# Kernel tuning notes

Hardware: AMD Instinct MI355X
Metric: run time of the kernel (lower is better)

Reference implementation:

```python
import jax, jax.numpy as jnp
import numpy as np

B, S, D = 2, 2048, 1024
QH, KVH, DH = 16, 4, 64
TOP_K = 128
ROPE_BASE = 10000.0


def _rope(x):
    # x: [B, H, S, DH]; standard LLaMA-style rotate-half RoPE, no freq scaling
    half = DH // 2
    inv_freq = 1.0 / (ROPE_BASE ** (jnp.arange(half, dtype=jnp.float32) / half))
    ang = jnp.arange(S, dtype=jnp.float32)[:, None] * inv_freq[None, :]  # [S, half]
    cos, sin = jnp.cos(ang), jnp.sin(ang)
    x1, x2 = x[..., :half], x[..., half:]
    return jnp.concatenate([x1 * cos - x2 * sin, x2 * cos + x1 * sin], axis=-1)


def setup_inputs() -> dict:
    key = jax.random.key(0)
    ks = jax.random.split(key, 5)
    return {
        "x": jax.random.normal(ks[0], (B, S, D), dtype=jnp.float32),
        "Wq": jax.random.normal(ks[1], (QH * DH, D), dtype=jnp.float32) * 0.02,
        "Wk": jax.random.normal(ks[2], (KVH * DH, D), dtype=jnp.float32) * 0.02,
        "Wv": jax.random.normal(ks[3], (KVH * DH, D), dtype=jnp.float32) * 0.02,
        "Wo": jax.random.normal(ks[4], (D, QH * DH), dtype=jnp.float32) * 0.02,
    }


def reference(x, Wq, Wk, Wv, Wo):
    # projections (Linear, no bias): y = x @ W.T
    q = (x @ Wq.T).reshape(B, S, QH, DH).transpose(0, 2, 1, 3)   # [B,QH,S,DH]
    k = (x @ Wk.T).reshape(B, S, KVH, DH).transpose(0, 2, 1, 3)  # [B,KVH,S,DH]
    v = (x @ Wv.T).reshape(B, S, KVH, DH).transpose(0, 2, 1, 3)
    q = _rope(q)
    k = _rope(k)
    # repeat_kv: GQA expand kv heads to q heads
    rep = QH // KVH
    k = jnp.repeat(k, rep, axis=1)
    v = jnp.repeat(v, rep, axis=1)
    scores = jnp.einsum("bhqd,bhkd->bhqk", q, k) / np.sqrt(DH)  # [B,QH,S,S]
    causal = jnp.triu(jnp.ones((S, S), dtype=bool), k=1)
    scores = jnp.where(causal, -jnp.inf, scores)
    # top-k masking before softmax: keep entries >= per-row k-th largest score
    top_vals = jax.lax.top_k(scores, TOP_K)[0]        # [B,QH,S,TOP_K]
    thr = top_vals[..., -1:]
    scores = jnp.where(scores < thr, -jnp.inf, scores)
    w = jax.nn.softmax(scores, axis=-1)
    out = jnp.einsum("bhqk,bhkd->bhqd", w, v)         # [B,QH,S,DH]
    out = out.transpose(0, 2, 1, 3).reshape(B, S, QH * DH)
    return out @ Wo.T
```

## Files before the change

kernel.cpp:

```cpp
#include <hip/hip_runtime.h>
#include <hip/hip_bf16.h>
#include <hip/hip_fp16.h>
#include <math.h>

constexpr int cB   = 2;
constexpr int cS   = 2048;
constexpr int cD   = 1024;
constexpr int cQH  = 16;
constexpr int cKVH = 4;
constexpr int cDH  = 64;
constexpr int cTOPK = 128;
constexpr int cM   = cB * cS;
constexpr int cNB  = cS / 64;
constexpr int cLSZ = 384;

constexpr int cTI  = 8;
constexpr int cSTR = 130;

constexpr int cNQ  = cQH * cDH;
constexpr int cNK  = cKVH * cDH;
constexpr int cNQKV = cNQ + 2 * cNK;

typedef __attribute__((ext_vector_type(8))) short short8;
typedef __attribute__((ext_vector_type(4))) float floatx4;
typedef _Float16 half8 __attribute__((ext_vector_type(8)));

__device__ inline ushort f2bf(float f) {
    unsigned u = __float_as_uint(f);
    return (ushort)((u + 0x7FFFu + ((u >> 16) & 1u)) >> 16);
}

__device__ __forceinline__ void glds16(const ushort* g, ushort* l) {
    __builtin_amdgcn_global_load_lds(
        (const __attribute__((address_space(1))) unsigned int*)g,
        (__attribute__((address_space(3))) unsigned int*)l, 16, 0, 0);
}

constexpr int cE0 = cM * cD;
constexpr int cE1 = cE0 + cNQ * cD;
constexpr int cE2 = cE1 + cNK * cD;
constexpr int cE3 = cE2 + cNK * cD;
constexpr int cE4 = cE3 + cD * cQH * cDH;

__global__ void cast_all_bf16(const float* __restrict__ x,
                              const float* __restrict__ wq,
                              const float* __restrict__ wk,
                              const float* __restrict__ wv,
                              const float* __restrict__ wo,
                              ushort* __restrict__ dst) {
    const int i4 = (blockIdx.x * blockDim.x + threadIdx.x) * 4;
    if (i4 >= cE4) return;
    const float* s;
    int off;
    if (i4 < cE0)      { s = x;  off = i4; }
    else if (i4 < cE1) { s = wq; off = i4 - cE0; }
    else if (i4 < cE2) { s = wk; off = i4 - cE1; }
    else if (i4 < cE3) { s = wv; off = i4 - cE2; }
    else               { s = wo; off = i4 - cE3; }
    const float4 v = *(const float4*)(s + off);
    ushort4 r;
    r.x = f2bf(v.x); r.y = f2bf(v.y); r.z = f2bf(v.z); r.w = f2bf(v.w);
    *(ushort4*)(dst + i4) = r;
}

__global__ __launch_bounds__(256) void gemm_bf16_bt(
        const ushort* __restrict__ A, const ushort* __restrict__ W,
        float* __restrict__ C, int M, int N, int K) {
    __shared__ ushort AsL[128 * 32];
    __shared__ ushort BsL[128 * 32];

    const int tid  = threadIdx.x;
    const int lane = tid & 63;
    const int w    = tid >> 6;
    const int wm   = (w & 1) * 64;
    const int wn   = (w >> 1) * 64;
    const int m0   = blockIdx.y * 128;
    const int n0   = blockIdx.x * 128;
    const int quad = lane >> 4;
    const int l16  = lane & 15;

    int r0, q0, r1, q1;
    {
        const int g5 = (w * 128 + lane) & 31;
        const int b4 = (g5 >> 4) & 1, b3 = (g5 >> 3) & 1, b2 = (g5 >> 2) & 1;
        const int b1 = (g5 >> 1) & 1, b0 = g5 & 1;
        r0 = ((w * 128 + lane) >> 5) * 8 + ((b4 << 2) | (b3 << 1) | (b2 ^ b4));
        q0 = ((b1 ^ b3) << 1) | (b0 ^ b2 ^ b4);
    }
    {
        const int gI = w * 128 + 64 + lane;
        const int g5 = gI & 31;
        const int b4 = (g5 >> 4) & 1, b3 = (g5 >> 3) & 1, b2 = (g5 >> 2) & 1;
        const int b1 = (g5 >> 1) & 1, b0 = g5 & 1;
        r1 = (gI >> 5) * 8 + ((b4 << 2) | (b3 << 1) | (b2 ^ b4));
        q1 = ((b1 ^ b3) << 1) | (b0 ^ b2 ^ b4);
    }
    const size_t aOff0 = (size_t)(m0 + r0) * K + q0 * 8;
    const size_t aOff1 = (size_t)(m0 + r1) * K + q1 * 8;
    const size_t bOff0 = (size_t)(n0 + r0) * K + q0 * 8;
    const size_t bOff1 = (size_t)(n0 + r1) * K + q1 * 8;
    ushort* ldsA0 = AsL + w * 1024;
    ushort* ldsA1 = AsL + w * 1024 + 512;
    ushort* ldsB0 = BsL + w * 1024;
    ushort* ldsB1 = BsL + w * 1024 + 512;

    int eA[4], eB[4];
    #pragma unroll
    for (int mi = 0; mi < 4; ++mi) {
        const int rr = wm + mi * 16 + l16;
        eA[mi] = (((rr >> 3) * 32) + ((4 * (rr & 7) + quad) ^ (rr & 7))) * 8;
    }
    #pragma unroll
    for (int ni = 0; ni < 4; ++ni) {
        const int rn = wn + ni * 16 + l16;
        eB[ni] = (((rn >> 3) * 32) + ((4 * (rn & 7) + quad) ^ (rn & 7))) * 8;
    }

    floatx4 acc[4][4];
    #pragma unroll
    for (int mi = 0; mi < 4; ++mi)
        #pragma unroll
        for (int ni = 0; ni < 4; ++ni)
            acc[mi][ni] = (floatx4){0.f, 0.f, 0.f, 0.f};

    for (int k0 = 0; k0 < K; k0 += 32) {
        glds16(A + aOff0 + k0, ldsA0);
        glds16(A + aOff1 + k0, ldsA1);
        glds16(W + bOff0 + k0, ldsB0);
        glds16(W + bOff1 + k0, ldsB1);
        __syncthreads();

        short8 af[4], bf[4];
        #pragma unroll
        for (int mi = 0; mi < 4; ++mi)
            af[mi] = *(const short8*)(AsL + eA[mi]);
        #pragma unroll
        for (int ni = 0; ni < 4; ++ni)
            bf[ni] = *(const short8*)(BsL + eB[ni]);
        #pragma unroll
        for (int mi = 0; mi < 4; ++mi)
            #pragma unroll
            for (int ni = 0; ni < 4; ++ni)
                acc[mi][ni] = __builtin_amdgcn_mfma_f32_16x16x32_bf16(
                    af[mi], bf[ni], acc[mi][ni], 0, 0, 0);
        __syncthreads();
    }

    #pragma unroll
    for (int mi = 0; mi < 4; ++mi)
        #pragma unroll
        for (int ni = 0; ni < 4; ++ni)
            #pragma unroll
            for (int r = 0; r < 4; ++r) {
                const int row = m0 + wm + mi * 16 + quad * 4 + r;
                const int col = n0 + wn + ni * 16 + l16;
                C[(size_t)row * N + col] = acc[mi][ni][r];
            }
}

__global__ void rope_cast_f16(const float* __restrict__ src,
                              ushort* __restrict__ dst, int H, int total,
                              float scale, int srcStride) {
    int idx = blockIdx.x * blockDim.x + threadIdx.x;
    if (idx >= total) return;
    const int d   = idx & 31;
    const int h   = (idx >> 5) % H;
    const int row = idx / (32 * H);
    const int s   = row % cS;
    const float inv_freq = powf(10000.0f, -(float)d / 32.0f);
    const float ang = (float)s * inv_freq;
    const float c  = cosf(ang);
    const float si = sinf(ang);
    const float* p = src + (size_t)row * srcStride + (size_t)h * cDH;
    const float x1 = p[d];
    const float x2 = p[d + 32];
    const float r1 = (x1 * c - x2 * si) * scale;
    const float r2 = (x2 * c + x1 * si) * scale;
    ushort* o = dst + (size_t)row * H * cDH + (size_t)h * cDH;
    o[d]      = __builtin_bit_cast(ushort, (_Float16)r1);
    o[d + 32] = __builtin_bit_cast(ushort, (_Float16)r2);
}

__global__ void cast_f32_f16_strided(const float* __restrict__ src,
                                     ushort* __restrict__ dst,
                                     int total, int cols, int srcStride) {
    const int i4 = (blockIdx.x * blockDim.x + threadIdx.x) * 4;
    if (i4 >= total) return;
    const int row = i4 / cols;
    const int col = i4 - row * cols;
    const float4 v = *(const float4*)(src + (size_t)row * srcStride + col);
    ushort4 r;
    r.x = __builtin_bit_cast(ushort, (_Float16)v.x);
    r.y = __builtin_bit_cast(ushort, (_Float16)v.y);
    r.z = __builtin_bit_cast(ushort, (_Float16)v.z);
    r.w = __builtin_bit_cast(ushort, (_Float16)v.w);
    *(ushort4*)(dst + i4) = r;
}

__device__ inline unsigned fmap(float f) {
    unsigned u = __float_as_uint(f);
    return (u & 0x80000000u) ? ~u : (u | 0x80000000u);
}
__device__ inline float funmap(unsigned u) {
    unsigned v = (u & 0x80000000u) ? (u & 0x7FFFFFFFu) : ~u;
    return __uint_as_float(v);
}

__global__ __launch_bounds__(512) void attn_tile_kernel(
        const ushort* __restrict__ qf, const ushort* __restrict__ kf,
        const ushort* __restrict__ vf, ushort* __restrict__ out) {
    extern __shared__ char smem[];
    unsigned* stg = (unsigned*)smem;
    unsigned* klA = (unsigned*)smem;
    int*      jlA = (int*)(klA + cTI * cLSZ);

    const int lane = threadIdx.x & 63;
    const int wv   = __builtin_amdgcn_readfirstlane(threadIdx.x >> 6);

    const int x  = blockIdx.x;
    const int it = (cS / cTI - 1) - (x >> 5);
    const int bh = x & 31;
    const int h  = bh & 15;
    const int b  = bh >> 4;
    const int kvh = h >> 2;
    const int i0  = it * cTI;

    const size_t bS = (size_t)b * cS;
    const int l16   = lane & 15;
    const int quad  = lane >> 4;
    const int jperm = ((lane & 3) << 4) + (lane >> 2);
    const int i     = i0 + wv;

    const ushort* qp = qf + ((bS + i0 + (l16 & 7)) * cQH + h) * cDH + quad * 8;
    const half8 a0h = __builtin_bit_cast(half8, *(const uint4*)qp);
    const half8 a1h = __builtin_bit_cast(half8, *(const uint4*)(qp + 32));

    unsigned key[cNB];
    #pragma unroll
    for (int jb = 0; jb < cNB; ++jb) key[jb] = 0u;

    const int nk16   = ((i0 + cTI - 1) >> 4) + 1;
    const int nchunk = (nk16 + 7) >> 3;

    uint4 pb0, pb1;
    if (wv < nk16) {
        const ushort* kp = kf + ((bS + (wv << 4) + l16) * cKVH + kvh) * cDH + quad * 8;
        pb0 = *(const uint4*)kp;
        pb1 = *(const uint4*)(kp + 32);
    }

    #pragma unroll
    for (int c = 0; c < 16; ++c) {
        if (c >= nchunk) break;
        const int  kb16  = (c << 3) + wv;
        const bool valid = (kb16 < nk16);
        const uint4 b0 = pb0, b1 = pb1;
        const int  kb16n = ((c + 1) << 3) + wv;
        if (kb16n < nk16) {
            const ushort* kp = kf + ((bS + (kb16n << 4) + l16) * cKVH + kvh) * cDH + quad * 8;
            pb0 = *(const uint4*)kp;
            pb1 = *(const uint4*)(kp + 32);
        }
        if (valid) {
            floatx4 acc = (floatx4){0.f, 0.f, 0.f, 0.f};
            acc = __builtin_amdgcn_mfma_f32_16x16x32_f16(
                a0h, __builtin_bit_cast(half8, b0), acc, 0, 0, 0);
            acc = __builtin_amdgcn_mfma_f32_16x16x32_f16(
                a1h, __builtin_bit_cast(half8, b1), acc, 0, 0, 0);
            if (quad < 2) {
                unsigned* sp = stg + (c & 1) * (cTI * cSTR) + (wv << 4) + l16;
                #pragma unroll
                for (int r2 = 0; r2 < 4; ++r2)
                    sp[(quad * 4 + r2) * cSTR] = __float_as_uint(acc[r2]);
            }
        }
        __syncthreads();
        {
            const unsigned* rp = stg + (c & 1) * (cTI * cSTR) + wv * cSTR;
            #pragma unroll
            for (int jj = 0; jj < 2; ++jj) {
                const int j = (c << 7) + (jj << 6) + jperm;
                const unsigned kr = rp[(jj << 6) + jperm];
                key[(c << 1) + jj] =
                    (j <= i) ? fmap(__uint_as_float(kr)) : 0u;
            }
        }
    }
    __syncthreads();

    const int nb = (i >> 6) + 1;
    unsigned* kl = klA + wv * cLSZ;
    int*      jl = jlA + wv * cLSZ;
    const int vbase0 = (int)(((unsigned)bS * cKVH + kvh) * cDH);

    unsigned um = 0u, un = 0xFFFFFFFFu;
    #pragma unroll
    for (int jb = 0; jb < cNB; ++jb) {
        if (jb >= nb) break;
        const unsigned kk = key[jb];
        um = max(um, kk);
        un = min(un, kk ? kk : 0xFFFFFFFFu);
    }
    #pragma unroll
    for (int off = 32; off >= 1; off >>= 1) {
        um = max(um, (unsigned)__shfl_xor((int)um, off));
        un = min(un, (unsigned)__shfl_xor((int)un, off));
    }
    const float mrow = funmap(um);

    unsigned ustar;
    if (i < cTOPK) {
        ustar = un;
    } else {
        unsigned lo = un, hi = um;
        while (lo < hi) {
            const unsigned d   = hi - lo;
            const unsigned mid = lo + (d >> 1) + (d & 1u);
            int cnt2 = 0;
            #pragma unroll
            for (int jb = 0; jb < cNB; ++jb) {
                if (jb >= nb) break;
                cnt2 += __popcll(__ballot(key[jb] >= mid));
            }
            if (cnt2 == cTOPK) {
                unsigned mn = 0xFFFFFFFFu;
                #pragma unroll
                for (int jb = 0; jb < cNB; ++jb) {
                    if (jb >= nb) break;
                    const unsigned kk = key[jb];
                    mn = min(mn, (kk >= mid) ? kk : 0xFFFFFFFFu);
                }
                #pragma unroll
                for (int off = 32; off >= 1; off >>= 1)
                    mn = min(mn, (unsigned)__shfl_xor((int)mn, off));
                lo = mn;
                break;
            }
            if (cnt2 > cTOPK) lo = mid; else hi = mid - 1u;
        }
        ustar = lo;
    }

    const unsigned long long mlt = (1ull << lane) - 1ull;
    int base = 0;
    #pragma unroll
    for (int jb = 0; jb < cNB; ++jb) {
        if (jb >= nb) break;
        const int j = (jb << 6) + jperm;
        const bool keep = (j <= i) && (key[jb] >= ustar);
        const unsigned long long mk = __ballot(keep);
        const int pos = base + __popcll(mk & mlt);
        if (keep && pos < cLSZ) {
            kl[pos] = key[jb];
            jl[pos] = vbase0 + j * (cKVH * cDH);
        }
        base += __popcll(mk);
    }
    const int cnt = min(base, cLSZ);

    float zp = 0.f;
    for (int t = lane; t < cnt; t += 64) {
        const float s  = funmap(kl[t]);
        const float wt = __expf(s - mrow);
        ((float*)kl)[t] = wt;
        zp += wt;
    }
    #pragma unroll
    for (int off = 32; off >= 1; off >>= 1) zp += __shfl_xor(zp, off);
    const float invZ = 1.0f / zp;

    float ac0 = 0.f, ac1 = 0.f, ac2 = 0.f, ac3 = 0.f;
    float ac4 = 0.f, ac5 = 0.f, ac6 = 0.f, ac7 = 0.f;
    int t = 0;
    #pragma unroll 2
    for (; t + 7 < cnt; t += 8) {
        const float wt0 = ((float*)kl)[t];
        const float wt1 = ((float*)kl)[t + 1];
        const float wt2 = ((float*)kl)[t + 2];
        const float wt3 = ((float*)kl)[t + 3];
        const float wt4 = ((float*)kl)[t + 4];
        const float wt5 = ((float*)kl)[t + 5];
        const float wt6 = ((float*)kl)[t + 6];
        const float wt7 = ((float*)kl)[t + 7];
        const int vo0 = jl[t];
        const int vo1 = jl[t + 1];
        const int vo2 = jl[t + 2];
        const int vo3 = jl[t + 3];
        const int vo4 = jl[t + 4];
        const int vo5 = jl[t + 5];
        const int vo6 = jl[t + 6];
        const int vo7 = jl[t + 7];
        ac0 += wt0 * (float)__builtin_bit_cast(_Float16, vf[vo0 + lane]);
        ac1 += wt1 * (float)__builtin_bit_cast(_Float16, vf[vo1 + lane]);
        ac2 += wt2 * (float)__builtin_bit_cast(_Float16, vf[vo2 + lane]);
        ac3 += wt3 * (float)__builtin_bit_cast(_Float16, vf[vo3 + lane]);
        ac4 += wt4 * (float)__builtin_bit_cast(_Float16, vf[vo4 + lane]);
        ac5 += wt5 * (float)__builtin_bit_cast(_Float16, vf[vo5 + lane]);
        ac6 += wt6 * (float)__builtin_bit_cast(_Float16, vf[vo6 + lane]);
        ac7 += wt7 * (float)__builtin_bit_cast(_Float16, vf[vo7 + lane]);
    }
    for (; t < cnt; ++t) {
        const float wt = ((float*)kl)[t];
        const int   vo = jl[t];
        ac0 += wt * (float)__builtin_bit_cast(_Float16, vf[vo + lane]);
    }
    const float acc = ((ac0 + ac1) + (ac2 + ac3)) + ((ac4 + ac5) + (ac6 + ac7));
    out[((bS + i) * cQH + h) * cDH + lane] = f2bf(acc * invZ);
}

extern "C" void kernel_launch(void* const* d_in, const int* in_sizes, int n_in,
                              void* d_out, int out_size, void* d_ws, size_t ws_size,
                              hipStream_t stream) {
    const float* x  = (const float*)d_in[0];
    const float* Wq = (const float*)d_in[1];
    const float* Wk = (const float*)d_in[2];
    const float* Wv = (const float*)d_in[3];
    const float* Wo = (const float*)d_in[4];
    float* out = (float*)d_out;

    float*  qkvb = (float*)d_ws;
    ushort* xh   = (ushort*)(qkvb + (size_t)cM * cNQKV);
    ushort* Wqh  = xh  + (size_t)cM * cD;
    ushort* Wkh  = Wqh + (size_t)cNQ * cD;
    ushort* Wvh  = Wkh + (size_t)cNK * cD;
    ushort* Woh  = Wvh + (size_t)cNK * cD;
    ushort* abh  = Woh + (size_t)cD * cQH * cDH;
    ushort* qff  = abh + (size_t)cM * cQH * cDH;
    ushort* kff  = qff + (size_t)cM * cQH * cDH;
    ushort* vff  = kff + (size_t)cM * cKVH * cDH;

    dim3 blk(256);

    cast_all_bf16<<<(cE4 / 4 + 255) / 256, blk, 0, stream>>>(
        x, Wq, Wk, Wv, Wo, xh);

    gemm_bf16_bt<<<dim3(cNQKV / 128, cM / 128), blk, 0, stream>>>(
        xh, Wqh, qkvb, cM, cNQKV, cD);

    {
        const int totq = cM * cQH * 32;
        const int totk = cM * cKVH * 32;
        rope_cast_f16<<<(totq + 255) / 256, blk, 0, stream>>>(
            qkvb, qff, cQH, totq, 0.125f, cNQKV);
        rope_cast_f16<<<(totk + 255) / 256, blk, 0, stream>>>(
            qkvb + cNQ, kff, cKVH, totk, 1.0f, cNQKV);
        const int nv = cM * cNK;
        cast_f32_f16_strided<<<(nv / 4 + 255) / 256, blk, 0, stream>>>(
            qkvb + cNQ + cNK, vff, nv, cNK, cNQKV);
    }

    constexpr size_t aSMEM = (size_t)cTI * cLSZ * 8;
    static_assert(2 * cTI * cSTR * 4 <= (int)aSMEM, "staging must fit");
    attn_tile_kernel<<<dim3(32 * (cS / cTI)), dim3(512), aSMEM, stream>>>(
        qff, kff, vff, abh);

    gemm_bf16_bt<<<dim3(cD / 128, cM / 128), blk, 0, stream>>>(abh, Woh, out, cM, cD, cD);
}
```

Before: 534.9 us.

## Double attention query tile to 16 rows and precompute RoPE trig table

Grows the attention tile from 8 to 16 query rows per block, with 1024 threads, so each 16x16 MFMA score tile uses all 16 query rows instead of duplicating 8. It also moves the causal mask and the key mapping into the score-staging write, and drops the software prefetch of K fragments. Separately, a small kernel builds cos/sin tables once so the RoPE kernels read them instead of calling powf/sin/cos per element. The larger blocks halve the grid count and may reduce occupancy or raise register pressure. Losing the K prefetch may expose load latency.

Measured after the change: 520.4 us. 2.7% less time.

```diff
diff --git a/kernel.cpp b/kernel.cpp
--- a/kernel.cpp
+++ b/kernel.cpp
@@ -14,8 +14,8 @@
 constexpr int cNB  = cS / 64;
 constexpr int cLSZ = 384;
 
-constexpr int cTI  = 8;
-constexpr int cSTR = 130;
+constexpr int cTI  = 16;
+constexpr int cSTR = 258;
 
 constexpr int cNQ  = cQH * cDH;
 constexpr int cNK  = cKVH * cDH;
@@ -63,6 +63,17 @@
     *(ushort4*)(dst + i4) = r;
 }
 
+__global__ void build_trig(float* __restrict__ ct, float* __restrict__ st) {
+    const int idx = blockIdx.x * blockDim.x + threadIdx.x;
+    if (idx >= cS * 32) return;
+    const int d = idx & 31;
+    const int s = idx >> 5;
+    const float inv_freq = powf(10000.0f, -(float)d / 32.0f);
+    const float ang = (float)s * inv_freq;
+    ct[idx] = cosf(ang);
+    st[idx] = sinf(ang);
+}
+
 __global__ __launch_bounds__(256) void gemm_bf16_bt(
         const ushort* __restrict__ A, const ushort* __restrict__ W,
         float* __restrict__ C, int M, int N, int K) {
@@ -160,17 +171,17 @@
 
 __global__ void rope_cast_f16(const float* __restrict__ src,
                               ushort* __restrict__ dst, int H, int total,
-                              float scale, int srcStride) {
+                              float scale, int srcStride,
+                              const float* __restrict__ ct,
+                              const float* __restrict__ st) {
     int idx = blockIdx.x * blockDim.x + threadIdx.x;
     if (idx >= total) return;
     const int d   = idx & 31;
     const int h   = (idx >> 5) % H;
     const int row = idx / (32 * H);
     const int s   = row % cS;
-    const float inv_freq = powf(10000.0f, -(float)d / 32.0f);
-    const float ang = (float)s * inv_freq;
-    const float c  = cosf(ang);
-    const float si = sinf(ang);
+    const float c  = ct[(s << 5) + d];
+    const float si = st[(s << 5) + d];
     const float* p = src + (size_t)row * srcStride + (size_t)h * cDH;
     const float x1 = p[d];
     const float x2 = p[d + 32];
@@ -206,7 +217,7 @@
     return __uint_as_float(v);
 }
 
-__global__ __launch_bounds__(512) void attn_tile_kernel(
+__global__ __launch_bounds__(1024) void attn_tile_kernel(
         const ushort* __restrict__ qf, const ushort* __restrict__ kf,
         const ushort* __restrict__ vf, ushort* __restrict__ out) {
     extern __shared__ char smem[];
@@ -231,7 +242,7 @@
     const int jperm = ((lane & 3) << 4) + (lane >> 2);
     const int i     = i0 + wv;
 
-    const ushort* qp = qf + ((bS + i0 + (l16 & 7)) * cQH + h) * cDH + quad * 8;
+    const ushort* qp = qf + ((bS + i0 + l16) * cQH + h) * cDH + quad * 8;
     const half8 a0h = __builtin_bit_cast(half8, *(const uint4*)qp);
     const half8 a1h = __builtin_bit_cast(half8, *(const uint4*)(qp + 32));
 
@@ -239,50 +250,38 @@
     #pragma unroll
     for (int jb = 0; jb < cNB; ++jb) key[jb] = 0u;
 
-    const int nk16   = ((i0 + cTI - 1) >> 4) + 1;
-    const int nchunk = (nk16 + 7) >> 3;
-
-    uint4 pb0, pb1;
-    if (wv < nk16) {
-        const ushort* kp = kf + ((bS + (wv << 4) + l16) * cKVH + kvh) * cDH + quad * 8;
-        pb0 = *(const uint4*)kp;
-        pb1 = *(const uint4*)(kp + 32);
-    }
-
-    #pragma unroll
-    for (int c = 0; c < 16; ++c) {
+    const int nk16   = it + 1;
+    const int nchunk = (nk16 + 15) >> 4;
+
+    #pragma unroll
+    for (int c = 0; c < 8; ++c) {
         if (c >= nchunk) break;
-        const int  kb16  = (c << 3) + wv;
-        const bool valid = (kb16 < nk16);
-        const uint4 b0 = pb0, b1 = pb1;
-        const int  kb16n = ((c + 1) << 3) + wv;
-        if (kb16n < nk16) {
-            const ushort* kp = kf + ((bS + (kb16n << 4) + l16) * cKVH + kvh) * cDH + quad * 8;
-            pb0 = *(const uint4*)kp;
-            pb1 = *(const uint4*)(kp + 32);
-        }
-        if (valid) {
+        const int kb16 = (c << 4) + wv;
+        if (kb16 < nk16) {
+            const ushort* kp = kf + ((bS + (kb16 << 4) + l16) * cKVH + kvh) * cDH + quad * 8;
+            const uint4 b0 = *(const uint4*)kp;
+            const uint4 b1 = *(const uint4*)(kp + 32);
             floatx4 acc = (floatx4){0.f, 0.f, 0.f, 0.f};
             acc = __builtin_amdgcn_mfma_f32_16x16x32_f16(
                 a0h, __builtin_bit_cast(half8, b0), acc, 0, 0, 0);
             acc = __builtin_amdgcn_mfma_f32_16x16x32_f16(
                 a1h, __builtin_bit_cast(half8, b1), acc, 0, 0, 0);
-            if (quad < 2) {
-                unsigned* sp = stg + (c & 1) * (cTI * cSTR) + (wv << 4) + l16;
-                #pragma unroll
-                for (int r2 = 0; r2 < 4; ++r2)
-                    sp[(quad * 4 + r2) * cSTR] = __float_as_uint(acc[r2]);
+            const int jg = (kb16 << 4) + l16;
+            unsigned* sp = stg + (c & 1) * (cTI * cSTR) + (wv << 4) + l16;
+            #pragma unroll
+            for (int r2 = 0; r2 < 4; ++r2) {
+                const int qrow = quad * 4 + r2;
+                sp[qrow * cSTR] = (jg <= i0 + qrow) ? fmap(acc[r2]) : 0u;
             }
         }
         __syncthreads();
         {
             const unsigned* rp = stg + (c & 1) * (cTI * cSTR) + wv * cSTR;
             #pragma unroll
-            for (int jj = 0; jj < 2; ++jj) {
-                const int j = (c << 7) + (jj << 6) + jperm;
+            for (int jj = 0; jj < 4; ++jj) {
+                const int j = (c << 8) + (jj << 6) + jperm;
                 const unsigned kr = rp[(jj << 6) + jperm];
-                key[(c << 1) + jj] =
-                    (j <= i) ? fmap(__uint_as_float(kr)) : 0u;
+                key[(c << 2) + jj] = (j <= i) ? kr : 0u;
             }
         }
     }
@@ -428,11 +427,15 @@
     ushort* qff  = abh + (size_t)cM * cQH * cDH;
     ushort* kff  = qff + (size_t)cM * cQH * cDH;
     ushort* vff  = kff + (size_t)cM * cKVH * cDH;
+    float*  ct   = (float*)(vff + (size_t)cM * cKVH * cDH);
+    float*  st   = ct + (size_t)cS * 32;
 
     dim3 blk(256);
 
     cast_all_bf16<<<(cE4 / 4 + 255) / 256, blk, 0, stream>>>(
         x, Wq, Wk, Wv, Wo, xh);
+
+    build_trig<<<(cS * 32 + 255) / 256, blk, 0, stream>>>(ct, st);
 
     gemm_bf16_bt<<<dim3(cNQKV / 128, cM / 128), blk, 0, stream>>>(
         xh, Wqh, qkvb, cM, cNQKV, cD);
@@ -441,9 +444,9 @@
         const int totq = cM * cQH * 32;
         const int totk = cM * cKVH * 32;
         rope_cast_f16<<<(totq + 255) / 256, blk, 0, stream>>>(
-            qkvb, qff, cQH, totq, 0.125f, cNQKV);
+            qkvb, qff, cQH, totq, 0.125f, cNQKV, ct, st);
         rope_cast_f16<<<(totk + 255) / 256, blk, 0, stream>>>(
-            qkvb + cNQ, kff, cKVH, totk, 1.0f, cNQKV);
+            qkvb + cNQ, kff, cKVH, totk, 1.0f, cNQKV, ct, st);
         const int nv = cM * cNK;
         cast_f32_f16_strided<<<(nv / 4 + 255) / 256, blk, 0, stream>>>(
             qkvb + cNQ + cNK, vff, nv, cNK, cNQKV);
@@ -451,7 +454,7 @@
 
     constexpr size_t aSMEM = (size_t)cTI * cLSZ * 8;
     static_assert(2 * cTI * cSTR * 4 <= (int)aSMEM, "staging must fit");
-    attn_tile_kernel<<<dim3(32 * (cS / cTI)), dim3(512), aSMEM, stream>>>(
+    attn_tile_kernel<<<dim3(32 * (cS / cTI)), dim3(1024), aSMEM, stream>>>(
         qff, kff, vff, abh);
 
     gemm_bf16_bt<<<dim3(cD / 128, cM / 128), blk, 0, stream>>>(abh, Woh, out, cM, cD, cD);
```
